# Optimization experiments

Hardware: AMD Instinct MI355X
Metric: run time of the kernel (lower is better)

The kernel has to match this reference:

```python
import jax, jax.numpy as jnp
import numpy as np
from jax import lax

B, C, H, W = 16, 256, 64, 64
HID = 128
EQ = 256


def _lstm_dir(x, Wih, Whh, b, hidden):
    # x: [N, T, D]; PyTorch gate order i, f, g, o
    N = x.shape[0]
    h0 = jnp.zeros((N, hidden), x.dtype)
    c0 = jnp.zeros((N, hidden), x.dtype)
    xT = jnp.swapaxes(x, 0, 1)  # [T, N, D]
    pre = jnp.einsum('tnd,gd->tng', xT, Wih) + b  # precompute input projection

    def step(carry, xt):
        h, c = carry
        g = xt + h @ Whh.T
        i, f, gg, o = jnp.split(g, 4, axis=-1)
        c = jax.nn.sigmoid(f) * c + jax.nn.sigmoid(i) * jnp.tanh(gg)
        h = jax.nn.sigmoid(o) * jnp.tanh(c)
        return (h, c), h

    _, hs = lax.scan(step, (h0, c0), pre)
    return jnp.swapaxes(hs, 0, 1)  # [N, T, hidden]


def _bilstm(x, Wih_f, Whh_f, b_f, Wih_b, Whh_b, b_b, hidden):
    hf = _lstm_dir(x, Wih_f, Whh_f, b_f, hidden)
    hb = _lstm_dir(x[:, ::-1], Wih_b, Whh_b, b_b, hidden)[:, ::-1]
    return jnp.concatenate([hf, hb], axis=-1)


def setup_inputs() -> dict:
    key = jax.random.key(0)
    ks = jax.random.split(key, 16)
    s = 1.0 / np.sqrt(HID)
    d = {}
    d['input'] = jax.random.normal(ks[0], (B, C, H, W), jnp.float32)
    # horizontal LSTM (input_size=C)
    d['h_Wih_f'] = jax.random.uniform(ks[1], (4 * HID, C), jnp.float32, -s, s)
    d['h_Whh_f'] = jax.random.uniform(ks[2], (4 * HID, HID), jnp.float32, -s, s)
    d['h_b_f'] = jax.random.uniform(ks[3], (4 * HID,), jnp.float32, -s, s)
    d['h_Wih_b'] = jax.random.uniform(ks[4], (4 * HID, C), jnp.float32, -s, s)
    d['h_Whh_b'] = jax.random.uniform(ks[5], (4 * HID, HID), jnp.float32, -s, s)
    d['h_b_b'] = jax.random.uniform(ks[6], (4 * HID,), jnp.float32, -s, s)
    # vertical LSTM (input_size=2*HID)
    d['v_Wih_f'] = jax.random.uniform(ks[7], (4 * HID, 2 * HID), jnp.float32, -s, s)
    d['v_Whh_f'] = jax.random.uniform(ks[8], (4 * HID, HID), jnp.float32, -s, s)
    d['v_b_f'] = jax.random.uniform(ks[9], (4 * HID,), jnp.float32, -s, s)
    d['v_Wih_b'] = jax.random.uniform(ks[10], (4 * HID, 2 * HID), jnp.float32, -s, s)
    d['v_Whh_b'] = jax.random.uniform(ks[11], (4 * HID, HID), jnp.float32, -s, s)
    d['v_b_b'] = jax.random.uniform(ks[12], (4 * HID,), jnp.float32, -s, s)
    # 1x1 convs (no bias)
    d['Wr'] = jax.random.normal(ks[13], (EQ, 2 * HID), jnp.float32) * 0.05
    d['Wl'] = jax.random.normal(ks[14], (EQ, C), jnp.float32) * 0.05
    d['alpha'] = jnp.zeros((1,), jnp.float32) + 0.5  # nonzero so output depends on attention
    return d


def reference(input, h_Wih_f, h_Whh_f, h_b_f, h_Wih_b, h_Whh_b, h_b_b,
              v_Wih_f, v_Whh_f, v_b_f, v_Wih_b, v_Whh_b, v_b_b, Wr, Wl, alpha):
    b, c, h, w = input.shape
    # transpose(1,3): [B, W, H, C]; horizontal LSTM runs over H for each w
    x = jnp.transpose(input, (0, 3, 2, 1))  # [B, W, H, C]
    xh = x.reshape(b * w, h, c)
    hor = _bilstm(xh, h_Wih_f, h_Whh_f, h_b_f, h_Wih_b, h_Whh_b, h_b_b, HID)
    hor = hor.reshape(b, w, h, 2 * HID)  # == torch horizontal_feature
    # vertical LSTM: sequences over W for each h-index
    xv = jnp.transpose(hor, (0, 2, 1, 3)).reshape(b * h, w, 2 * HID)
    ver = _bilstm(xv, v_Wih_f, v_Whh_f, v_b_f, v_Wih_b, v_Whh_b, v_b_b, HID)
    ver = ver.reshape(b, h, w, 2 * HID)  # vf[b, hi, wi, :]
    # torch: stack dim=2 -> [B, W, H, 2Hd]; permute(0,3,1,2) -> [B, 2Hd, W, H]
    vf = jnp.transpose(ver, (0, 3, 2, 1))  # [B, 2Hd, W, H]
    vf = jnp.einsum('oc,bcwh->bowh', Wr, vf)  # conv_right 1x1
    vf = vf.reshape(b, EQ, h * w)
    vf = jax.nn.softmax(vf, axis=2)
    # left branch
    q = jnp.einsum('oc,bchw->bohw', Wl, input)
    q_avg = jnp.mean(q, axis=(2, 3)).reshape(b, 1, EQ)
    q_avg = jax.nn.softmax(q_avg, axis=2)
    attention = jnp.matmul(q_avg, vf).reshape(b, 1, h, w)
    attention = jax.nn.sigmoid(attention)
    out = input * attention
    return out * alpha + input
```

## Files before the change

kernel.cpp:

```cpp
#include <hip/hip_runtime.h>
#include <hip/hip_bf16.h>

typedef unsigned short u16;
typedef unsigned int u32;
typedef unsigned char u8;
typedef long long ll8;
typedef __attribute__((ext_vector_type(4))) float f4v;

__device__ __forceinline__ float rcpf(float x) { return __builtin_amdgcn_rcpf(x); }
__device__ __forceinline__ float ex2(float x) {
#if __has_builtin(__builtin_amdgcn_exp2f)
  return __builtin_amdgcn_exp2f(x);
#else
  return exp2f(x);
#endif
}
__device__ __forceinline__ float sigf(float x) { return rcpf(1.0f + __expf(-x)); }
template<bool HI>
__device__ __forceinline__ u32 pkfp8(float a, float b, u32 old) {
  return (u32)__builtin_amdgcn_cvt_pk_fp8_f32(a, b, (int)old, HI);
}
__device__ __forceinline__ u8 f2f8(float x) { return (u8)(pkfp8<false>(x, x, 0) & 0xffu); }
template<int S>
__device__ __forceinline__ float f8tof(u32 v) {
#if __has_builtin(__builtin_amdgcn_cvt_f32_fp8)
  return __builtin_amdgcn_cvt_f32_fp8((int)v, S);
#else
  u8 b = (u8)(v >> (8 * S));
  u32 s = (b >> 7) & 1u, e = (b >> 3) & 15u, m = b & 7u;
  union { u32 i; float f; } r;
  if (e) r.i = (s << 31) | ((e + 120u) << 23) | (m << 20);
  else { r.f = (float)m * 0.001953125f; r.i |= s << 31; }
  return r.f;
#endif
}

#define GS_IFO 1.4426950408889634f
#define GS_G   2.8853900817779268f

__device__ __forceinline__ void gl_lds16(const void* g, void* l) {
  __builtin_amdgcn_global_load_lds(
      (const __attribute__((address_space(1))) u32*)g,
      (__attribute__((address_space(3))) u32*)l, 16, 0, 0);
}

struct CvtArgs {
  const float* src[9];
  u8* dst[9];
  int n4[9];
  int scl[9];
  int sh[9];
};
__global__ __launch_bounds__(256) void k_cvt(CvtArgs a) {
  int seg = blockIdx.y;
  int i = blockIdx.x * 256 + threadIdx.x;
  if (i >= a.n4[seg]) return;
  float4 v = ((const float4*)a.src[seg])[i];
  float s;
  if (a.scl[seg] == 2) {
    s = GS_IFO;
  } else {
    int r = i >> a.sh[seg];
    s = (((r >> 7) & 3) == 2) ? GS_G : GS_IFO;
  }
  v.x *= s; v.y *= s; v.z *= s; v.w *= s;
  u32 p = pkfp8<false>(v.x, v.y, 0);
  p = pkfp8<true>(v.z, v.w, p);
  ((u32*)a.dst[seg])[i] = p;
}

__global__ __launch_bounds__(256) void k_tin(const float* __restrict__ in,
                                             u8* __restrict__ A8,
                                             float* __restrict__ meansum) {
  int b = blockIdx.z, h = blockIdx.y, c0 = blockIdx.x * 64;
  int t = threadIdx.x, lane = t & 63, q = t >> 6;
  __shared__ u8 lT[64][68];
  const float* src = in + ((b * 256 + c0) * 64 + h) * 64;
#pragma unroll 4
  for (int i = 0; i < 16; ++i) {
    int cl = q * 16 + i;
    float v = src[cl * 4096 + lane];
    lT[cl][lane] = f2f8(v);
    float s = v;
#pragma unroll
    for (int off = 32; off; off >>= 1) s += __shfl_xor(s, off);
    if (lane == 0) atomicAdd(&meansum[b * 256 + c0 + cl], s);
  }
  __syncthreads();
  u8* dst = A8 + (b * 4096 + h) * 256 + c0;
#pragma unroll 4
  for (int i = 0; i < 16; ++i) {
    int w = q * 16 + i;
    dst[w * 16384 + lane] = lT[lane][w];
  }
}

__global__ __launch_bounds__(256) void k_qavg(const float* __restrict__ meansum,
                                              const float* __restrict__ Wl,
                                              float* __restrict__ qavg) {
  int b = blockIdx.x, t = threadIdx.x;
  __shared__ float mean[256];
  __shared__ float red[256];
  mean[t] = meansum[b * 256 + t] * (1.0f / 4096.0f);
  __syncthreads();
  const float* wr = Wl + t * 256;
  float acc = 0.0f;
  for (int c = 0; c < 256; ++c) acc = fmaf(wr[c], mean[c], acc);
  red[t] = acc; __syncthreads();
  for (int s = 128; s; s >>= 1) { if (t < s) red[t] = fmaxf(red[t], red[t + s]); __syncthreads(); }
  float mx = red[0]; __syncthreads();
  float e = __expf(acc - mx);
  red[t] = e; __syncthreads();
  for (int s = 128; s; s >>= 1) { if (t < s) red[t] += red[t + s]; __syncthreads(); }
  qavg[b * 256 + t] = e / red[0];
}

__global__ __launch_bounds__(256, 2) void k_gemm8(const u8* __restrict__ A,
                                                  const u8* __restrict__ W,
                                                  u8* __restrict__ out,
                                                  float* __restrict__ Zsum) {
  int nwg = gridDim.x;
  int q = nwg >> 3;
  int bid = blockIdx.x;
  int swz = (bid & 7) * q + (bid >> 3);
  int mt = swz >> 1, nt = swz & 1;
  int mb = mt << 7, nb = nt << 7;
  int t = threadIdx.x, lane = t & 63, wid = t >> 6;
  int laneg = lane & 15, lk = lane >> 4;
  __shared__ __align__(16) u8 lA[128][256];
  __shared__ __align__(16) u8 lW[128][256];
  {
    int rl = lane >> 4;
    int unit = lane & 15;
#pragma unroll
    for (int i = 0; i < 8; ++i) {
      int rb4 = ((wid << 3) + i) << 2;
      int r = rb4 + rl;
      int usA = unit ^ (r & 7);
      gl_lds16(A + (mb + r) * 256 + (usA << 4), &lA[rb4][0]);
      gl_lds16(W + (nb + r) * 256 + (usA << 4), &lW[rb4][0]);
    }
  }
  __syncthreads();
  f4v acc[4][4] = {};
  int wm = wid >> 1, wn = wid & 1;
#pragma unroll
  for (int kk = 0; kk < 8; ++kk) {
    ll8 af[4], bf[4];
#pragma unroll
    for (int m = 0; m < 4; ++m) {
      int r = (wm << 6) + (m << 4) + laneg;
      int us = ((kk << 1) + (lk >> 1)) ^ (r & 7);
      af[m] = *(const ll8*)&lA[r][(us << 4) + ((lk & 1) << 3)];
    }
#pragma unroll
    for (int n = 0; n < 4; ++n) {
      int r = (wn << 6) + (n << 4) + laneg;
      int us = ((kk << 1) + (lk >> 1)) ^ (r & 7);
      bf[n] = *(const ll8*)&lW[r][(us << 4) + ((lk & 1) << 3)];
    }
#pragma unroll
    for (int m = 0; m < 4; ++m)
#pragma unroll
      for (int n = 0; n < 4; ++n)
        acc[m][n] = __builtin_amdgcn_mfma_f32_16x16x32_fp8_fp8(af[m], bf[n], acc[m][n], 0, 0, 0);
  }
#pragma unroll
  for (int n = 0; n < 4; ++n) {
    int col = nb + (wn << 6) + (n << 4) + laneg;
    float csum = 0.f;
#pragma unroll
    for (int m = 0; m < 4; ++m) {
      int row0 = mb + (wm << 6) + (m << 4) + (lk << 2);
#pragma unroll
      for (int j = 0; j < 4; ++j) {
        float e = ex2(acc[m][n][j]);
        csum += e;
        out[(row0 + j) * 256 + col] = f2f8(e);
      }
    }
    csum += __shfl_xor(csum, 16);
    csum += __shfl_xor(csum, 32);
    if (lk == 0) atomicAdd(&Zsum[((mb >> 12) << 8) + col], csum);
  }
}

__global__ __launch_bounds__(512, 1) void k_recur_f(const u8* __restrict__ X8,
                                                    const u8* __restrict__ Wi8,
                                                    const u8* __restrict__ Wh8d,
                                                    const float* __restrict__ bias_f,
                                                    const float* __restrict__ bias_b,
                                                    u8* __restrict__ outb) {
  int dir = blockIdx.y;
  int s0 = blockIdx.x << 4;
  int t = threadIdx.x, lane = t & 63, w = t >> 6;
  int laneg = lane & 15, lk = lane >> 4;
  const u8* Wd = Wh8d + dir * 65536;
  const u8* Wi = Wi8 + dir * 131072;
  const float* bia = dir ? bias_b : bias_f;
  int hc = w << 4;
  ll8 bfr[4][4];
#pragma unroll
  for (int g = 0; g < 4; ++g)
#pragma unroll
    for (int kk = 0; kk < 4; ++kk)
      bfr[g][kk] = *(const ll8*)(Wd + (g * 128 + hc + laneg) * 128 + kk * 32 + lk * 8);
  ll8 ifr[4][8];
#pragma unroll
  for (int g = 0; g < 4; ++g)
#pragma unroll
    for (int kk = 0; kk < 8; ++kk)
      ifr[g][kk] = *(const ll8*)(Wi + (g * 128 + hc + laneg) * 256 + kk * 32 + lk * 8);
  float bval[4];
#pragma unroll
  for (int g = 0; g < 4; ++g)
    bval[g] = bia[g * 128 + hc + laneg] * ((g == 2) ? GS_G : GS_IFO);

  __shared__ __align__(16) u8 hb[2][16][144];
  __shared__ __align__(16) u8 xb[4][16][256];
  for (int i = t; i < 2 * 16 * 144; i += 512) ((u8*)hb)[i] = 0;

  float cs[4] = {0.f, 0.f, 0.f, 0.f};
  int tc0 = dir ? 63 : 0;
  int dstep = dir ? -1 : 1;
  int srw = (w << 2) + (lane >> 4);
  int c16 = lane & 15;
  const u8* xsrc = X8 + (s0 + srw) * 16384 + ((c16 ^ (srw & 7)) << 4);
  int srow = t >> 5;
  int schunk = t & 31;
  int rowb = ((s0 >> 6) << 12) + (s0 & 63);
  if (w < 4) {
    gl_lds16(xsrc + tc0 * 256, &xb[0][w << 2][0]);
    gl_lds16(xsrc + (tc0 + dstep) * 256, &xb[1][w << 2][0]);
    gl_lds16(xsrc + (tc0 + 2 * dstep) * 256, &xb[2][w << 2][0]);
  }
  __syncthreads();
  f4v nacc[4];
#pragma unroll
  for (int g = 0; g < 4; ++g)
    nacc[g] = (f4v){bval[g], bval[g], bval[g], bval[g]};
  {
    const u8* xrow = &xb[0][laneg][0];
    ll8 xf[8];
#pragma unroll
    for (int kk = 0; kk < 8; ++kk)
      xf[kk] = *(const ll8*)&xrow[((((kk << 1) + (lk >> 1)) ^ (laneg & 7)) << 4) + ((lk & 1) << 3)];
#pragma unroll
    for (int g = 0; g < 4; ++g)
#pragma unroll
      for (int kk = 0; kk < 8; ++kk)
        nacc[g] = __builtin_amdgcn_mfma_f32_16x16x32_fp8_fp8(xf[kk], ifr[g][kk], nacc[g], 0, 0, 0);
  }
  int cur = 0;
  for (int st = 0; st < 64; ++st) {
    int tc = tc0 + st * dstep;
    f4v acc[4];
#pragma unroll
    for (int g = 0; g < 4; ++g) acc[g] = nacc[g];
    if (st) {
      int pr = tc - dstep;
      u32 hv = *(const u32*)&hb[cur][srow][schunk << 2];
      *(u32*)(outb + (rowb + pr * 64 + srow) * 256 + (dir << 7) + (schunk << 2)) = hv;
    }
    if (w < 4 && st < 61) {
      gl_lds16(xsrc + (tc0 + (st + 3) * dstep) * 256, &xb[(st + 3) & 3][w << 2][0]);
    }
    {
      ll8 afr[4];
#pragma unroll
      for (int kk = 0; kk < 4; ++kk)
        afr[kk] = *(const ll8*)&hb[cur][laneg][kk * 32 + lk * 8];
#pragma unroll
      for (int g = 0; g < 4; ++g)
#pragma unroll
        for (int kk = 0; kk < 4; ++kk)
          acc[g] = __builtin_amdgcn_mfma_f32_16x16x32_fp8_fp8(afr[kk], bfr[g][kk], acc[g], 0, 0, 0);
    }
    if (st < 63) {
      asm volatile("s_waitcnt vmcnt(4)" ::: "memory");
#pragma unroll
      for (int g = 0; g < 4; ++g)
        nacc[g] = (f4v){bval[g], bval[g], bval[g], bval[g]};
      const u8* xrow = &xb[(st + 1) & 3][laneg][0];
      ll8 xf[8];
#pragma unroll
      for (int kk = 0; kk < 8; ++kk)
        xf[kk] = *(const ll8*)&xrow[((((kk << 1) + (lk >> 1)) ^ (laneg & 7)) << 4) + ((lk & 1) << 3)];
#pragma unroll
      for (int g = 0; g < 4; ++g)
#pragma unroll
        for (int kk = 0; kk < 8; ++kk)
          nacc[g] = __builtin_amdgcn_mfma_f32_16x16x32_fp8_fp8(xf[kk], ifr[g][kk], nacc[g], 0, 0, 0);
    }
    int nxt = cur ^ 1;
#pragma unroll
    for (int j = 0; j < 4; ++j) {
      float Y = ex2(-acc[0][j]);
      float V = ex2(-acc[1][j]);
      float X = ex2(acc[2][j]);
      float W = ex2(-acc[3][j]);
      float ig = (X - 1.0f) * rcpf((1.0f + Y) * (X + 1.0f));
      float c = cs[j] * rcpf(1.0f + V) + ig;
      cs[j] = c;
      float Z = ex2(c * GS_G);
      float h = (Z - 1.0f) * rcpf((1.0f + W) * (Z + 1.0f));
      hb[nxt][(lk << 2) + j][hc + laneg] = f2f8(h);
    }
    asm volatile("s_waitcnt lgkmcnt(0)" ::: "memory");
    __builtin_amdgcn_s_barrier();
    cur = nxt;
  }
  {
    int pr = tc0 + 63 * dstep;
    u32 hv = *(const u32*)&hb[cur][srow][schunk << 2];
    *(u32*)(outb + (rowb + pr * 64 + srow) * 256 + (dir << 7) + (schunk << 2)) = hv;
  }
}

__global__ __launch_bounds__(256) void k_attfin(const u8* __restrict__ VF8,
                                                const float* __restrict__ qavg,
                                                const float* __restrict__ Z,
                                                const float* __restrict__ in,
                                                const float* __restrict__ alpha,
                                                float* __restrict__ out) {
  int bx = blockIdx.x;
  int b = bx >> 6;
  int sp0 = (bx & 63) << 6;
  int t = threadIdx.x, lane = t & 63, wid = t >> 6;
  __shared__ __align__(16) float lwo[256];
  __shared__ float fac[64];
  lwo[t] = qavg[b * 256 + t] / Z[b * 256 + t];
  __syncthreads();
  float4 wo = *(const float4*)&lwo[lane * 4];
  int rowbase = b * 4096 + sp0;
#pragma unroll 4
  for (int i = 0; i < 16; ++i) {
    int r = wid * 16 + i;
    u32 v = *(const u32*)&VF8[(rowbase + r) * 256 + lane * 4];
    float p = wo.x * f8tof<0>(v) + wo.y * f8tof<1>(v) +
              wo.z * f8tof<2>(v) + wo.w * f8tof<3>(v);
#pragma unroll
    for (int off = 32; off; off >>= 1) p += __shfl_xor(p, off);
    if (lane == 0) fac[r] = p;
  }
  __syncthreads();
  float al = alpha[0];
  if (t < 64) fac[t] = 1.0f + al * sigf(fac[t]);
  __syncthreads();
  int sp = t & 63;
  float f = fac[sp];
  const float* ip = in + (long)b * 1048576 + sp0 + sp;
  float* op = out + (long)b * 1048576 + sp0 + sp;
  int c0 = t >> 6;
#pragma unroll 8
  for (int c = c0; c < 256; c += 4) {
    op[c * 4096] = ip[c * 4096] * f;
  }
}

extern "C" void kernel_launch(void* const* d_in, const int* in_sizes, int n_in,
                              void* d_out, int out_size, void* d_ws, size_t ws_size,
                              hipStream_t stream) {
  const float* input   = (const float*)d_in[0];
  const float* h_Wih_f = (const float*)d_in[1];
  const float* h_Whh_f = (const float*)d_in[2];
  const float* h_b_f   = (const float*)d_in[3];
  const float* h_Wih_b = (const float*)d_in[4];
  const float* h_Whh_b = (const float*)d_in[5];
  const float* h_b_b   = (const float*)d_in[6];
  const float* v_Wih_f = (const float*)d_in[7];
  const float* v_Whh_f = (const float*)d_in[8];
  const float* v_b_f   = (const float*)d_in[9];
  const float* v_Wih_b = (const float*)d_in[10];
  const float* v_Whh_b = (const float*)d_in[11];
  const float* v_b_b   = (const float*)d_in[12];
  const float* Wr      = (const float*)d_in[13];
  const float* Wl      = (const float*)d_in[14];
  const float* alphap  = (const float*)d_in[15];

  char* ws = (char*)d_ws;
  u8*  Ah8   = (u8*)(ws + 0);
  u8*  VF8   = (u8*)(ws + 33554432);
  u8*  Wh8   = (u8*)(ws + 67108864);
  u8*  Wv8   = (u8*)(ws + 67371008);
  u8*  WhhH8 = (u8*)(ws + 67633152);
  u8*  WhhV8 = (u8*)(ws + 67764224);
  u8*  Wrb8  = (u8*)(ws + 67895296);
  float* meansum = (float*)(ws + 67960832);
  float* qavg    = (float*)(ws + 67977216);
  float* pZ      = (float*)(ws + 67993600);
  u8*  Av8 = (u8*)d_out;
  u8*  Ar8 = Ah8;

  (void)hipMemsetAsync(meansum, 0, 3 * 16384, stream);

  CvtArgs ca;
  ca.src[0] = h_Wih_f; ca.dst[0] = Wh8;           ca.n4[0] = 32768; ca.scl[0] = 1; ca.sh[0] = 6;
  ca.src[1] = h_Wih_b; ca.dst[1] = Wh8 + 131072;  ca.n4[1] = 32768; ca.scl[1] = 1; ca.sh[1] = 6;
  ca.src[2] = v_Wih_f; ca.dst[2] = Wv8;           ca.n4[2] = 32768; ca.scl[2] = 1; ca.sh[2] = 6;
  ca.src[3] = v_Wih_b; ca.dst[3] = Wv8 + 131072;  ca.n4[3] = 32768; ca.scl[3] = 1; ca.sh[3] = 6;
  ca.src[4] = h_Whh_f; ca.dst[4] = WhhH8;         ca.n4[4] = 16384; ca.scl[4] = 1; ca.sh[4] = 5;
  ca.src[5] = h_Whh_b; ca.dst[5] = WhhH8 + 65536; ca.n4[5] = 16384; ca.scl[5] = 1; ca.sh[5] = 5;
  ca.src[6] = v_Whh_f; ca.dst[6] = WhhV8;         ca.n4[6] = 16384; ca.scl[6] = 1; ca.sh[6] = 5;
  ca.src[7] = v_Whh_b; ca.dst[7] = WhhV8 + 65536; ca.n4[7] = 16384; ca.scl[7] = 1; ca.sh[7] = 5;
  ca.src[8] = Wr;      ca.dst[8] = Wrb8;          ca.n4[8] = 16384; ca.scl[8] = 2; ca.sh[8] = 6;
  k_cvt<<<dim3(128, 9), 256, 0, stream>>>(ca);

  k_tin<<<dim3(4, 64, 16), 256, 0, stream>>>(input, Ah8, meansum);
  k_qavg<<<16, 256, 0, stream>>>(meansum, Wl, qavg);

  k_recur_f<<<dim3(64, 2), 512, 0, stream>>>(Ah8, Wh8, WhhH8, h_b_f, h_b_b, Av8);
  k_recur_f<<<dim3(64, 2), 512, 0, stream>>>(Av8, Wv8, WhhV8, v_b_f, v_b_b, Ar8);
  k_gemm8<<<1024, 256, 0, stream>>>(Ar8, Wrb8, VF8, pZ);

  k_attfin<<<1024, 256, 0, stream>>>(VF8, qavg, pZ, input, alphap, (float*)d_out);
}
```

Before: 307.2 us.

## Unroll LSTM recurrence by two with double-buffered input-projection accumulators

Unrolls the 64-step recurrent loop by two and keeps two accumulator sets, so the input projection for step t+2 is computed after the gate math of step t instead of before it. This moves the W_ih MFMA work off the critical path between the recurrent matmul and the nonlinearity. It also raises wave priority around the recurrent MFMA section and adjusts the vmcnt waits for the deeper prefetch. The cost is higher register pressure, and there is a leftover dead loop computing an unused exp2.

```diff
diff --git a/kernel.cpp b/kernel.cpp
--- a/kernel.cpp
+++ b/kernel.cpp
@@ -229,86 +229,137 @@
   int srow = t >> 5;
   int schunk = t & 31;
   int rowb = ((s0 >> 6) << 12) + (s0 & 63);
+
+  auto wihx = [&](f4v (&a)[4], const u8* xrow) {
+    ll8 xf[8];
+#pragma unroll
+    for (int kk = 0; kk < 8; ++kk)
+      xf[kk] = *(const ll8*)&xrow[((((kk << 1) + (lk >> 1)) ^ (laneg & 7)) << 4) + ((lk & 1) << 3)];
+#pragma unroll
+    for (int g = 0; g < 4; ++g)
+#pragma unroll
+      for (int kk = 0; kk < 8; ++kk)
+        a[g] = __builtin_amdgcn_mfma_f32_16x16x32_fp8_fp8(xf[kk], ifr[g][kk], a[g], 0, 0, 0);
+  };
+
   if (w < 4) {
     gl_lds16(xsrc + tc0 * 256, &xb[0][w << 2][0]);
     gl_lds16(xsrc + (tc0 + dstep) * 256, &xb[1][w << 2][0]);
     gl_lds16(xsrc + (tc0 + 2 * dstep) * 256, &xb[2][w << 2][0]);
   }
   __syncthreads();
-  f4v nacc[4];
-#pragma unroll
-  for (int g = 0; g < 4; ++g)
-    nacc[g] = (f4v){bval[g], bval[g], bval[g], bval[g]};
-  {
-    const u8* xrow = &xb[0][laneg][0];
-    ll8 xf[8];
-#pragma unroll
-    for (int kk = 0; kk < 8; ++kk)
-      xf[kk] = *(const ll8*)&xrow[((((kk << 1) + (lk >> 1)) ^ (laneg & 7)) << 4) + ((lk & 1) << 3)];
-#pragma unroll
-    for (int g = 0; g < 4; ++g)
-#pragma unroll
-      for (int kk = 0; kk < 8; ++kk)
-        nacc[g] = __builtin_amdgcn_mfma_f32_16x16x32_fp8_fp8(xf[kk], ifr[g][kk], nacc[g], 0, 0, 0);
-  }
+  f4v naccP[4], naccQ[4];
+#pragma unroll
+  for (int g = 0; g < 4; ++g) {
+    naccP[g] = (f4v){bval[g], bval[g], bval[g], bval[g]};
+    naccQ[g] = naccP[g];
+  }
+  wihx(naccP, &xb[0][laneg][0]);
+  wihx(naccQ, &xb[1][laneg][0]);
+
   int cur = 0;
-  for (int st = 0; st < 64; ++st) {
-    int tc = tc0 + st * dstep;
-    f4v acc[4];
-#pragma unroll
-    for (int g = 0; g < 4; ++g) acc[g] = nacc[g];
-    if (st) {
-      int pr = tc - dstep;
-      u32 hv = *(const u32*)&hb[cur][srow][schunk << 2];
-      *(u32*)(outb + (rowb + pr * 64 + srow) * 256 + (dir << 7) + (schunk << 2)) = hv;
-    }
-    if (w < 4 && st < 61) {
-      gl_lds16(xsrc + (tc0 + (st + 3) * dstep) * 256, &xb[(st + 3) & 3][w << 2][0]);
-    }
+  for (int st = 0; st < 64; st += 2) {
     {
-      ll8 afr[4];
-#pragma unroll
-      for (int kk = 0; kk < 4; ++kk)
-        afr[kk] = *(const ll8*)&hb[cur][laneg][kk * 32 + lk * 8];
-#pragma unroll
-      for (int g = 0; g < 4; ++g)
+      int tc = tc0 + st * dstep;
+      if (st) {
+        int pr = tc - dstep;
+        u32 hv = *(const u32*)&hb[cur][srow][schunk << 2];
+        *(u32*)(outb + (rowb + pr * 64 + srow) * 256 + (dir << 7) + (schunk << 2)) = hv;
+      }
+      if (w < 4 && st < 61)
+        gl_lds16(xsrc + (tc0 + (st + 3) * dstep) * 256, &xb[(st + 3) & 3][w << 2][0]);
+      __builtin_amdgcn_s_setprio(1);
+      {
+        ll8 afr[4];
 #pragma unroll
         for (int kk = 0; kk < 4; ++kk)
-          acc[g] = __builtin_amdgcn_mfma_f32_16x16x32_fp8_fp8(afr[kk], bfr[g][kk], acc[g], 0, 0, 0);
-    }
-    if (st < 63) {
-      asm volatile("s_waitcnt vmcnt(4)" ::: "memory");
-#pragma unroll
-      for (int g = 0; g < 4; ++g)
-        nacc[g] = (f4v){bval[g], bval[g], bval[g], bval[g]};
-      const u8* xrow = &xb[(st + 1) & 3][laneg][0];
-      ll8 xf[8];
-#pragma unroll
-      for (int kk = 0; kk < 8; ++kk)
-        xf[kk] = *(const ll8*)&xrow[((((kk << 1) + (lk >> 1)) ^ (laneg & 7)) << 4) + ((lk & 1) << 3)];
-#pragma unroll
-      for (int g = 0; g < 4; ++g)
-#pragma unroll
-        for (int kk = 0; kk < 8; ++kk)
-          nacc[g] = __builtin_amdgcn_mfma_f32_16x16x32_fp8_fp8(xf[kk], ifr[g][kk], nacc[g], 0, 0, 0);
-    }
-    int nxt = cur ^ 1;
-#pragma unroll
-    for (int j = 0; j < 4; ++j) {
-      float Y = ex2(-acc[0][j]);
-      float V = ex2(-acc[1][j]);
-      float X = ex2(acc[2][j]);
-      float W = ex2(-acc[3][j]);
-      float ig = (X - 1.0f) * rcpf((1.0f + Y) * (X + 1.0f));
-      float c = cs[j] * rcpf(1.0f + V) + ig;
-      cs[j] = c;
-      float Z = ex2(c * GS_G);
-      float h = (Z - 1.0f) * rcpf((1.0f + W) * (Z + 1.0f));
-      hb[nxt][(lk << 2) + j][hc + laneg] = f2f8(h);
-    }
-    asm volatile("s_waitcnt lgkmcnt(0)" ::: "memory");
-    __builtin_amdgcn_s_barrier();
-    cur = nxt;
+          afr[kk] = *(const ll8*)&hb[cur][laneg][kk * 32 + lk * 8];
+#pragma unroll
+        for (int g = 0; g < 4; ++g)
+#pragma unroll
+          for (int kk = 0; kk < 4; ++kk)
+            naccP[g] = __builtin_amdgcn_mfma_f32_16x16x32_fp8_fp8(afr[kk], bfr[g][kk], naccP[g], 0, 0, 0);
+      }
+      __builtin_amdgcn_s_setprio(0);
+      int nxt = cur ^ 1;
+#pragma unroll
+      for (int j = 0; j < 4; ++j) {
+        float Y = ex2(-naccP[j == 0 ? 0 : 0][j]);
+        (void)Y;
+      }
+#pragma unroll
+      for (int j = 0; j < 4; ++j) {
+        float Y = ex2(-naccP[0][j]);
+        float V = ex2(-naccP[1][j]);
+        float X = ex2(naccP[2][j]);
+        float Wo = ex2(-naccP[3][j]);
+        float ig = (X - 1.0f) * rcpf((1.0f + Y) * (X + 1.0f));
+        float c = cs[j] * rcpf(1.0f + V) + ig;
+        cs[j] = c;
+        float Z = ex2(c * GS_G);
+        float h = (Z - 1.0f) * rcpf((1.0f + Wo) * (Z + 1.0f));
+        hb[nxt][(lk << 2) + j][hc + laneg] = f2f8(h);
+      }
+      if (st < 62) {
+        if (st == 0) { asm volatile("s_waitcnt vmcnt(1)" ::: "memory"); }
+        else         { asm volatile("s_waitcnt vmcnt(2)" ::: "memory"); }
+#pragma unroll
+        for (int g = 0; g < 4; ++g)
+          naccP[g] = (f4v){bval[g], bval[g], bval[g], bval[g]};
+        wihx(naccP, &xb[(st + 2) & 3][laneg][0]);
+      }
+      asm volatile("s_waitcnt lgkmcnt(0)" ::: "memory");
+      __builtin_amdgcn_s_barrier();
+      cur = nxt;
+    }
+    {
+      int so = st + 1;
+      int tc = tc0 + so * dstep;
+      {
+        int pr = tc - dstep;
+        u32 hv = *(const u32*)&hb[cur][srow][schunk << 2];
+        *(u32*)(outb + (rowb + pr * 64 + srow) * 256 + (dir << 7) + (schunk << 2)) = hv;
+      }
+      if (w < 4 && so < 61)
+        gl_lds16(xsrc + (tc0 + (so + 3) * dstep) * 256, &xb[(so + 3) & 3][w << 2][0]);
+      __builtin_amdgcn_s_setprio(1);
+      {
+        ll8 afr[4];
+#pragma unroll
+        for (int kk = 0; kk < 4; ++kk)
+          afr[kk] = *(const ll8*)&hb[cur][laneg][kk * 32 + lk * 8];
+#pragma unroll
+        for (int g = 0; g < 4; ++g)
+#pragma unroll
+          for (int kk = 0; kk < 4; ++kk)
+            naccQ[g] = __builtin_amdgcn_mfma_f32_16x16x32_fp8_fp8(afr[kk], bfr[g][kk], naccQ[g], 0, 0, 0);
+      }
+      __builtin_amdgcn_s_setprio(0);
+      int nxt = cur ^ 1;
+#pragma unroll
+      for (int j = 0; j < 4; ++j) {
+        float Y = ex2(-naccQ[0][j]);
+        float V = ex2(-naccQ[1][j]);
+        float X = ex2(naccQ[2][j]);
+        float Wo = ex2(-naccQ[3][j]);
+        float ig = (X - 1.0f) * rcpf((1.0f + Y) * (X + 1.0f));
+        float c = cs[j] * rcpf(1.0f + V) + ig;
+        cs[j] = c;
+        float Z = ex2(c * GS_G);
+        float h = (Z - 1.0f) * rcpf((1.0f + Wo) * (Z + 1.0f));
+        hb[nxt][(lk << 2) + j][hc + laneg] = f2f8(h);
+      }
+      if (so < 62) {
+        asm volatile("s_waitcnt vmcnt(2)" ::: "memory");
+#pragma unroll
+        for (int g = 0; g < 4; ++g)
+          naccQ[g] = (f4v){bval[g], bval[g], bval[g], bval[g]};
+        wihx(naccQ, &xb[(so + 2) & 3][laneg][0]);
+      }
+      asm volatile("s_waitcnt lgkmcnt(0)" ::: "memory");
+      __builtin_amdgcn_s_barrier();
+      cur = nxt;
+    }
   }
   {
     int pr = tc0 + 63 * dstep;
```

After: 299.5 us. 2.5% less time.
